# Kernel tuning notes

Hardware: AMD Instinct MI355X
Metric: run time of the kernel (lower is better)

Reference implementation:

```python
import jax, jax.numpy as jnp
import numpy as np

NUM_BBOX = 2
NUM_CLASSES = 20
NUM_GRID = 7
THR_CONF = 0.5
THR_NMS = 0.3
BATCH = 128


def setup_inputs() -> dict:
    key = jax.random.key(0)
    C = NUM_BBOX * 4 + NUM_BBOX + NUM_CLASSES  # 30
    p = jax.random.normal(key, (BATCH, NUM_GRID, NUM_GRID, C), dtype=jnp.float32)
    return {"p_yolo_ts4": p}


def _decode(p):
    B, S = p.shape[0], p.shape[1]
    sc = NUM_BBOX * 4
    conf = jax.nn.sigmoid(p[..., sc:sc + NUM_BBOX])          # [B,S,S,nb] objectness
    cls = jax.nn.sigmoid(p[..., sc + NUM_BBOX:])             # [B,S,S,nc]
    boxes = p[..., :sc].reshape(B, S, S, NUM_BBOX, 4)
    xy = jax.nn.sigmoid(boxes[..., :2])                      # cell-relative offsets
    col = jnp.arange(S, dtype=p.dtype)
    cx = (xy[..., 0] + col[None, None, :, None]) / NUM_GRID  # + col index (x)
    cy = (xy[..., 1] + col[None, :, None, None]) / NUM_GRID  # + row index (y)
    w, h = boxes[..., 2], boxes[..., 3]                      # raw wh, as in source
    ltrb = jnp.stack([cx - w / 2, cy - h / 2, cx + w / 2, cy + h / 2], axis=-1)
    labels = jnp.argmax(cls, axis=-1) + 1                    # [B,S,S]
    valid = conf > THR_CONF                                  # [B,S,S,nb]
    return ltrb, conf, labels, valid


def _pairwise_iou(b):
    lt = jnp.maximum(b[:, None, :2], b[None, :, :2])
    rb = jnp.minimum(b[:, None, 2:], b[None, :, 2:])
    wh = jnp.clip(rb - lt, 0.0)
    inter = wh[..., 0] * wh[..., 1]
    area = (b[:, 2] - b[:, 0]) * (b[:, 3] - b[:, 1])
    union = area[:, None] + area[None, :] - inter
    return inter / jnp.maximum(union, 1e-9)


def reference(p_yolo_ts4):
    p = p_yolo_ts4
    B, S = p.shape[0], p.shape[1]
    ltrb, conf, labels, valid = _decode(p)
    N = B * S * S * NUM_BBOX
    boxes = ltrb.reshape(N, 4)
    scores = conf.reshape(N)
    labs = jnp.broadcast_to(labels[..., None], (B, S, S, NUM_BBOX)).reshape(N)
    idsb = jnp.broadcast_to(jnp.arange(B)[:, None, None, None], (B, S, S, NUM_BBOX)).reshape(N)
    vmask = valid.reshape(N)
    # sort by score (invalid last); greedy NMS per (batch, label) group
    order = jnp.argsort(jnp.where(vmask, scores, -jnp.inf))[::-1]
    boxes_s = boxes[order]
    scores_s = scores[order]
    labs_s = labs[order]
    idsb_s = idsb[order]
    v_s = vmask[order]
    iou = _pairwise_iou(boxes_s)                              # [N,N]
    same = (idsb_s[:, None] == idsb_s[None, :]) & (labs_s[:, None] == labs_s[None, :])
    later = jnp.arange(N)[None, :] > jnp.arange(N)[:, None]
    sup_mat = (iou > THR_NMS) & same & later & v_s[None, :]

    def body(i, sup):
        keep_i = v_s[i] & jnp.logical_not(sup[i])
        return jnp.where(keep_i, sup | sup_mat[i], sup)

    sup = jax.lax.fori_loop(0, N, body, jnp.zeros((N,), dtype=bool))
    keep = v_s & jnp.logical_not(sup)
    # fixed-shape outputs in descending-score order; `keep` marks surviving boxes
    return idsb_s, boxes_s, labs_s, scores_s, keep
```

## Files before the change

### kernel.cpp

```cpp
#include <hip/hip_runtime.h>
#include <math.h>

#define NBATCH 128
#define S 7
#define CH 30
#define N 12544
#define PERB 98
#define NWORDS 196
#define NCHUNK 16
#define CLENMAX 784
#define POISON 0xAAAAAAAAu
#define THRNMS 0.3

__device__ __forceinline__ float sigf(float x) {
    float e = (float)exp(-(double)x);
    return 1.0f / (1.0f + e);
}

__global__ __launch_bounds__(256) void k_decode(
    const float* __restrict__ p,
    float4* __restrict__ box4,
    float* __restrict__ score,
    int* __restrict__ meta,
    unsigned long long* __restrict__ ballots,
    unsigned long long* __restrict__ vK,
    unsigned int* __restrict__ vrank,
    unsigned int* __restrict__ counter)
{
    int i    = blockIdx.x * 256 + threadIdx.x;
    int lane = threadIdx.x & 63;
    int j    = i & 1;
    int cell = i >> 1;
    int x = cell % S, y = (cell / S) % S;
    const float* pc = p + cell * CH;

    float tx = pc[j*4+0], ty = pc[j*4+1], tw = pc[j*4+2], th = pc[j*4+3];
    float craw = pc[8 + j];

    int cbase = 10 + j * 10;
    float best = sigf(pc[cbase]); int lab = j * 10;
    #pragma unroll
    for (int c = 1; c < 10; ++c) {
        float v = sigf(pc[cbase + c]);
        if (v > best) { best = v; lab = j * 10 + c; }
    }
    float obest = __shfl_xor(best, 1);
    int   olab  = __shfl_xor(lab, 1);
    float bestA = j ? obest : best;  int labA = j ? olab : lab;
    float bestB = j ? best  : obest; int labB = j ? lab  : olab;
    int label = (bestB > bestA ? labB : labA) + 1;

    float sx = sigf(tx), sy = sigf(ty);
    float cx = (sx + (float)x) / 7.0f;
    float cy = (sy + (float)y) / 7.0f;
    float hw = tw / 2.0f, hh = th / 2.0f;
    float l = cx - hw, t = cy - hh, r = cx + hw, bt = cy + hh;

    float sc = sigf(craw);
    bool valid = sc > 0.5f;

    box4[i]  = make_float4(l, t, r, bt);
    score[i] = sc;
    meta[i]  = label;

    unsigned long long vb = __ballot(valid);
    if (lane == 0) ballots[i >> 6] = vb;

    unsigned int wcnt = (unsigned int)__popcll(vb);
    unsigned int basec = 0;
    if (lane == 0 && wcnt) basec = atomicAdd(counter, wcnt);
    basec = __shfl(basec, 0);
    if (valid) {
        unsigned int slot = (basec - POISON)
                          + (unsigned int)__popcll(vb & ((1ull << lane) - 1ull));
        vK[slot] = ((unsigned long long)__float_as_uint(sc) << 32)
                   | (unsigned long long)(unsigned int)i;
        vrank[slot] = 0u;
    }
}

__global__ __launch_bounds__(256) void k_rankv(
    const unsigned long long* __restrict__ vK,
    const unsigned int* __restrict__ counter,
    unsigned int* __restrict__ vrank)
{
    __shared__ unsigned long long lk[CLENMAX];
    const unsigned int nv = counter[0] - POISON;
    if ((unsigned int)(blockIdx.x * 256) >= nv) return;
    unsigned int clen = (nv + NCHUNK - 1) / NCHUNK;
    unsigned int base = blockIdx.y * clen;
    if (base >= nv) return;
    unsigned int len = (nv - base < clen) ? nv - base : clen;

    for (unsigned int u = threadIdx.x; u < len; u += 256) lk[u] = vK[base + u];
    __syncthreads();

    unsigned int s = blockIdx.x * 256 + threadIdx.x;
    if (s < nv) {
        unsigned long long Ki = vK[s];
        unsigned int cnt = 0;
        for (unsigned int u = 0; u < len; ++u)
            cnt += (lk[u] > Ki) ? 1u : 0u;
        if (cnt) atomicAdd(&vrank[s], cnt);
    }
}

__global__ __launch_bounds__(256) void k_finish(
    const unsigned long long* __restrict__ vK,
    const unsigned int* __restrict__ counter,
    const unsigned int* __restrict__ vrank,
    const unsigned long long* __restrict__ ballots,
    const float4* __restrict__ box4,
    const float* __restrict__ score,
    const int* __restrict__ meta,
    float* __restrict__ out)
{
    const int b   = blockIdx.x;
    const int tid = threadIdx.x;
    __shared__ unsigned long long blds[NWORDS];
    __shared__ unsigned long long mK[PERB];
    __shared__ int mslot[PERB];
    __shared__ unsigned int cnt_sh;
    __shared__ float sbx[PERB][4];
    __shared__ int   slb[PERB], spos[PERB], sup[PERB];
    __shared__ float ssc[PERB];

    if (tid == 0) cnt_sh = 0u;
    if (tid < NWORDS) blds[tid] = ballots[tid];
    __syncthreads();

    const unsigned int nv = counter[0] - POISON;
    for (unsigned int s = tid; s < nv; s += 256) {
        unsigned long long K = vK[s];
        unsigned int idx = (unsigned int)(K & 0xFFFFFFFFull);
        if ((int)(idx / PERB) == b) {
            unsigned int m = atomicAdd(&cnt_sh, 1u);
            mK[m] = K; mslot[m] = (int)s;
        }
    }
    __syncthreads();
    const int kb = (int)cnt_sh;

    if (tid < kb) {
        unsigned long long Kt = mK[tid];
        int rk = 0;
        for (int u = 0; u < kb; ++u) rk += (mK[u] > Kt) ? 1 : 0;
        unsigned int idx = (unsigned int)(Kt & 0xFFFFFFFFull);
        float4 b4 = box4[idx];
        sbx[rk][0] = b4.x; sbx[rk][1] = b4.y; sbx[rk][2] = b4.z; sbx[rk][3] = b4.w;
        slb[rk]  = meta[idx];
        ssc[rk]  = score[idx];
        spos[rk] = (int)vrank[mslot[tid]];
        sup[rk]  = 0;
    }
    __syncthreads();

    for (int i = 0; i < kb; ++i) {
        __syncthreads();
        if (sup[i]) continue;
        float li = sbx[i][0], ti = sbx[i][1], ri = sbx[i][2], bi = sbx[i][3];
        float areai = (ri - li) * (bi - ti);
        int labi = slb[i];
        int jj = tid;
        if (jj > i && jj < kb && slb[jj] == labi) {
            float lj = sbx[jj][0], tj = sbx[jj][1], rj = sbx[jj][2], bj = sbx[jj][3];
            float lt0 = fmaxf(li, lj), lt1 = fmaxf(ti, tj);
            float rb0 = fminf(ri, rj), rb1 = fminf(bi, bj);
            float w = rb0 - lt0; if (w < 0.0f) w = 0.0f;
            float h = rb1 - lt1; if (h < 0.0f) h = 0.0f;
            float inter = w * h;
            float areaj = (rj - lj) * (bj - tj);
            float uni = areai + areaj - inter;
            double iou = (double)inter / fmax((double)uni, 1e-9);
            if (iou > THRNMS) sup[jj] = 1;
        }
    }
    __syncthreads();

    if (tid < kb) {
        int pos = spos[tid];
        out[pos] = (float)b;
        ((float4*)(out + N))[pos] =
            make_float4(sbx[tid][0], sbx[tid][1], sbx[tid][2], sbx[tid][3]);
        out[5*N + pos] = (float)slb[tid];
        out[6*N + pos] = ssc[tid];
        out[7*N + pos] = sup[tid] ? 0.0f : 1.0f;
    }

    if (tid < PERB) {
        int i = b * PERB + tid;
        bool validown = (blds[i >> 6] >> (i & 63)) & 1ull;
        if (!validown) {
            unsigned int vle = 0;
            int wmax = i >> 6;
            for (int w = 0; w < wmax; ++w) vle += (unsigned int)__popcll(blds[w]);
            vle += (unsigned int)__popcll(blds[wmax] & ((1ull << (i & 63)) - 1ull));
            unsigned int pos = (unsigned int)(N - 1 - i) + vle;
            out[pos] = (float)b;
            ((float4*)(out + N))[pos] = box4[i];
            out[5*N + pos] = (float)meta[i];
            out[6*N + pos] = score[i];
            out[7*N + pos] = 0.0f;
        }
    }
}

extern "C" void kernel_launch(void* const* d_in, const int* in_sizes, int n_in,
                              void* d_out, int out_size, void* d_ws, size_t ws_size,
                              hipStream_t stream)
{
    const float* p = (const float*)d_in[0];
    float* out = (float*)d_out;

    char* w = (char*)d_ws;
    float4* box4          = (float4*)w;               w += (size_t)N * 16;
    unsigned long long* vK = (unsigned long long*)w;  w += (size_t)N * 8;
    unsigned long long* ballots = (unsigned long long*)w; w += (size_t)NWORDS * 8;
    float* score          = (float*)w;                w += (size_t)N * 4;
    int* meta             = (int*)w;                  w += (size_t)N * 4;
    unsigned int* vrank   = (unsigned int*)w;         w += (size_t)N * 4;
    unsigned int* counter = (unsigned int*)w;         w += 4;

    k_decode<<<dim3(N / 256),    dim3(256), 0, stream>>>(p, box4, score, meta,
                                                         ballots, vK, vrank, counter);
    k_rankv <<<dim3(49, NCHUNK), dim3(256), 0, stream>>>(vK, counter, vrank);
    k_finish<<<dim3(NBATCH),     dim3(256), 0, stream>>>(vK, counter, vrank, ballots,
                                                         box4, score, meta, out);
}
```

Baseline: 86.18 us.

## Fuse global rank computation into per-batch finish kernel and drop class sigmoid

Removes the separate k_rankv kernel and its vrank buffer. Each per-batch block of k_finish now computes the global rank of its own valid boxes by streaming all valid keys through shared memory in chunks, with each thread handling up to two candidate keys. The class-score argmax now compares raw logits instead of sigmoid outputs, since sigmoid is monotonic. This saves a kernel launch and the global atomics, but every one of the 128 blocks now scans the full valid-key list, which adds redundant work and leaves only 128 blocks in flight.

```diff
diff --git a/kernel.cpp b/kernel.cpp
--- a/kernel.cpp
+++ b/kernel.cpp
@@ -7,8 +7,7 @@
 #define N 12544
 #define PERB 98
 #define NWORDS 196
-#define NCHUNK 16
-#define CLENMAX 784
+#define CHUNK 2048
 #define POISON 0xAAAAAAAAu
 #define THRNMS 0.3
 
@@ -24,7 +23,6 @@
     int* __restrict__ meta,
     unsigned long long* __restrict__ ballots,
     unsigned long long* __restrict__ vK,
-    unsigned int* __restrict__ vrank,
     unsigned int* __restrict__ counter)
 {
     int i    = blockIdx.x * 256 + threadIdx.x;
@@ -38,10 +36,10 @@
     float craw = pc[8 + j];
 
     int cbase = 10 + j * 10;
-    float best = sigf(pc[cbase]); int lab = j * 10;
+    float best = pc[cbase]; int lab = j * 10;
     #pragma unroll
     for (int c = 1; c < 10; ++c) {
-        float v = sigf(pc[cbase + c]);
+        float v = pc[cbase + c];
         if (v > best) { best = v; lab = j * 10 + c; }
     }
     float obest = __shfl_xor(best, 1);
@@ -75,40 +73,12 @@
                           + (unsigned int)__popcll(vb & ((1ull << lane) - 1ull));
         vK[slot] = ((unsigned long long)__float_as_uint(sc) << 32)
                    | (unsigned long long)(unsigned int)i;
-        vrank[slot] = 0u;
-    }
-}
-
-__global__ __launch_bounds__(256) void k_rankv(
-    const unsigned long long* __restrict__ vK,
-    const unsigned int* __restrict__ counter,
-    unsigned int* __restrict__ vrank)
-{
-    __shared__ unsigned long long lk[CLENMAX];
-    const unsigned int nv = counter[0] - POISON;
-    if ((unsigned int)(blockIdx.x * 256) >= nv) return;
-    unsigned int clen = (nv + NCHUNK - 1) / NCHUNK;
-    unsigned int base = blockIdx.y * clen;
-    if (base >= nv) return;
-    unsigned int len = (nv - base < clen) ? nv - base : clen;
-
-    for (unsigned int u = threadIdx.x; u < len; u += 256) lk[u] = vK[base + u];
-    __syncthreads();
-
-    unsigned int s = blockIdx.x * 256 + threadIdx.x;
-    if (s < nv) {
-        unsigned long long Ki = vK[s];
-        unsigned int cnt = 0;
-        for (unsigned int u = 0; u < len; ++u)
-            cnt += (lk[u] > Ki) ? 1u : 0u;
-        if (cnt) atomicAdd(&vrank[s], cnt);
     }
 }
 
 __global__ __launch_bounds__(256) void k_finish(
     const unsigned long long* __restrict__ vK,
     const unsigned int* __restrict__ counter,
-    const unsigned int* __restrict__ vrank,
     const unsigned long long* __restrict__ ballots,
     const float4* __restrict__ box4,
     const float* __restrict__ score,
@@ -119,27 +89,56 @@
     const int tid = threadIdx.x;
     __shared__ unsigned long long blds[NWORDS];
     __shared__ unsigned long long mK[PERB];
-    __shared__ int mslot[PERB];
     __shared__ unsigned int cnt_sh;
+    __shared__ unsigned int grank[PERB];
+    __shared__ unsigned long long lk[CHUNK];
     __shared__ float sbx[PERB][4];
     __shared__ int   slb[PERB], spos[PERB], sup[PERB];
     __shared__ float ssc[PERB];
 
     if (tid == 0) cnt_sh = 0u;
+    if (tid < PERB) grank[tid] = 0u;
     if (tid < NWORDS) blds[tid] = ballots[tid];
     __syncthreads();
 
     const unsigned int nv = counter[0] - POISON;
+
     for (unsigned int s = tid; s < nv; s += 256) {
         unsigned long long K = vK[s];
         unsigned int idx = (unsigned int)(K & 0xFFFFFFFFull);
         if ((int)(idx / PERB) == b) {
             unsigned int m = atomicAdd(&cnt_sh, 1u);
-            mK[m] = K; mslot[m] = (int)s;
+            mK[m] = K;
         }
     }
     __syncthreads();
     const int kb = (int)cnt_sh;
+
+    const int m1  = tid & 63;
+    const int sub = tid >> 6;
+    const bool two = (kb > 64);
+    unsigned long long Km1 = (m1 < kb) ? mK[m1] : ~0ull;
+    unsigned long long Km2 = (two && (m1 + 64) < kb) ? mK[m1 + 64] : ~0ull;
+    unsigned int c1 = 0, c2 = 0;
+    for (unsigned int base = 0; base < nv; base += CHUNK) {
+        unsigned int len = nv - base; if (len > CHUNK) len = CHUNK;
+        for (unsigned int u = tid; u < len; u += 256) lk[u] = vK[base + u];
+        __syncthreads();
+        if (two) {
+            for (unsigned int u = sub; u < len; u += 4) {
+                unsigned long long k = lk[u];
+                c1 += (k > Km1) ? 1u : 0u;
+                c2 += (k > Km2) ? 1u : 0u;
+            }
+        } else {
+            for (unsigned int u = sub; u < len; u += 4)
+                c1 += (lk[u] > Km1) ? 1u : 0u;
+        }
+        __syncthreads();
+    }
+    if (c1) atomicAdd(&grank[m1], c1);
+    if (c2) atomicAdd(&grank[m1 + 64], c2);
+    __syncthreads();
 
     if (tid < kb) {
         unsigned long long Kt = mK[tid];
@@ -150,7 +149,7 @@
         sbx[rk][0] = b4.x; sbx[rk][1] = b4.y; sbx[rk][2] = b4.z; sbx[rk][3] = b4.w;
         slb[rk]  = meta[idx];
         ssc[rk]  = score[idx];
-        spos[rk] = (int)vrank[mslot[tid]];
+        spos[rk] = (int)grank[tid];
         sup[rk]  = 0;
     }
     __syncthreads();
@@ -218,12 +217,10 @@
     unsigned long long* ballots = (unsigned long long*)w; w += (size_t)NWORDS * 8;
     float* score          = (float*)w;                w += (size_t)N * 4;
     int* meta             = (int*)w;                  w += (size_t)N * 4;
-    unsigned int* vrank   = (unsigned int*)w;         w += (size_t)N * 4;
     unsigned int* counter = (unsigned int*)w;         w += 4;
 
-    k_decode<<<dim3(N / 256),    dim3(256), 0, stream>>>(p, box4, score, meta,
-                                                         ballots, vK, vrank, counter);
-    k_rankv <<<dim3(49, NCHUNK), dim3(256), 0, stream>>>(vK, counter, vrank);
-    k_finish<<<dim3(NBATCH),     dim3(256), 0, stream>>>(vK, counter, vrank, ballots,
-                                                         box4, score, meta, out);
-}
+    k_decode<<<dim3(N / 256), dim3(256), 0, stream>>>(p, box4, score, meta,
+                                                      ballots, vK, counter);
+    k_finish<<<dim3(NBATCH),  dim3(256), 0, stream>>>(vK, counter, ballots,
+                                                      box4, score, meta, out);
+}
```

Result: slower. 156.2 us (+81.2%).
